# Kernel tuning notes

Measured on AMD Instinct MI355X. Metric: run time of the kernel, lower is better.

## Reference

```python
import jax, jax.numpy as jnp
import numpy as np

BINS = 10
MOMENTUM = 0.5


def setup_inputs() -> dict:
    key = jax.random.key(0)
    k1, k2 = jax.random.split(key)
    B, D = 4096, 512
    x = jax.random.normal(k1, (B, D), dtype=jnp.float32)
    targets = jax.random.randint(k2, (B,), 0, 100, dtype=jnp.int64)
    acc_sum = jnp.zeros((BINS,), dtype=jnp.float32)
    return {"x": x, "acc_sum": acc_sum, "targets": targets}


def reference(x, acc_sum, targets):
    bins, momentum = BINS, MOMENTUM
    B = x.shape[0]
    # bin edges: arange(bins+1)/bins, last edge bumped by 1e-6
    edges = jnp.arange(bins + 1, dtype=jnp.float32) / bins
    edges = edges.at[-1].add(1e-6)

    # F.normalize: x / max(||x||_2, 1e-12) row-wise
    norm = jnp.maximum(jnp.linalg.norm(x, axis=1, keepdims=True), 1e-12)
    xn = x / norm
    cos = xn @ xn.T  # [B, B]

    label = (targets[:, None] == targets[None, :]).astype(jnp.float32)  # [B, B]

    g = jnp.abs(cos - label).ravel()  # gradient-density statistic, in [0, 2]
    # bin index i such that edges[i] <= g < edges[i+1]
    idx = jnp.searchsorted(edges, g, side="right") - 1
    valid = (idx >= 0) & (idx < bins)  # g >= edges[-1] falls in no bin -> weight 0

    # fused histogram (replaces the 10-iteration mask loop)
    counts = jnp.bincount(jnp.where(valid, idx, bins), length=bins + 1)[:bins]
    counts = counts.astype(jnp.float32)

    tot = jnp.float32(B * B)
    acc_new = momentum * acc_sum + (1.0 - momentum) * counts  # EMA update (momentum > 0 path)
    w_bin = tot / (acc_new + 1e-6)  # per-bin weight

    weights = jnp.where(valid, w_bin[jnp.clip(idx, 0, bins - 1)], 0.0)
    valid_num = jnp.sum(counts)
    weights = jnp.where(valid_num > 0, weights / valid_num, weights)

    loss = jnp.mean((label.ravel() - cos.ravel()) ** 2 * weights)
    return loss
```

## Files before the change

kernel.cpp:

```cpp
#include <hip/hip_runtime.h>
#include <hip/hip_bf16.h>

typedef __bf16 bf16x8 __attribute__((ext_vector_type(8)));
typedef float f32x16 __attribute__((ext_vector_type(16)));

typedef __attribute__((address_space(1))) void GAS;
typedef __attribute__((address_space(3))) void LAS;
#define GLOAD16(gp, lp) __builtin_amdgcn_global_load_lds((GAS*)(gp), (LAS*)(lp), 16, 0, 0)

#define NB 4096
#define NDU 1024
#define NKT 16

__global__ __launch_bounds__(256) void nrm_split_k(const float* __restrict__ x,
                                                   __bf16* __restrict__ u,
                                                   float* __restrict__ stats) {
    if (blockIdx.x == 0 && threadIdx.x < 21) stats[threadIdx.x] = 0.0f;
    const int wid = threadIdx.x >> 6, lane = threadIdx.x & 63;
    const int row = blockIdx.x * 4 + wid;
    const float4* xr = reinterpret_cast<const float4*>(x + (size_t)row * 512);
    float4 v0 = xr[lane * 2 + 0];
    float4 v1 = xr[lane * 2 + 1];
    float xv[8] = {v0.x, v0.y, v0.z, v0.w, v1.x, v1.y, v1.z, v1.w};
    float ss = 0.0f;
#pragma unroll
    for (int j = 0; j < 8; ++j) ss += xv[j] * xv[j];
#pragma unroll
    for (int off = 32; off > 0; off >>= 1) ss += __shfl_xor(ss, off);
    const float rn = 1.0f / fmaxf(sqrtf(ss), 1e-12f);
    bf16x8 h, l;
#pragma unroll
    for (int j = 0; j < 8; ++j) {
        float xn = xv[j] * rn;
        __bf16 hb = (__bf16)xn;
        h[j] = hb;
        l[j] = (__bf16)(xn - (float)hb);
    }
    reinterpret_cast<bf16x8*>(u + (size_t)row * NDU)[lane] = h;
    reinterpret_cast<bf16x8*>(u + (size_t)row * NDU + 512)[lane] = l;
}

__global__ __launch_bounds__(512, 2) void gemm_stat_k(const __bf16* __restrict__ u,
                                                      const int* __restrict__ targets,
                                                      const float* __restrict__ acc_sum,
                                                      float* __restrict__ stats,
                                                      float* __restrict__ out) {
    __shared__ __align__(16) __bf16 lds[2][4][128 * 64];
    __shared__ int tgtR[256], tgtC[256];
    __shared__ float red_s[8][10], red_c[8][10];

    const int bid = blockIdx.x;
    const int swz = (bid & 7) * 32 + (bid >> 3);
    const int by = swz >> 4, bx = swz & 15;
    const int row0 = by * 256, col0 = bx * 256;
    const int tid = threadIdx.x, lane = tid & 63;
    const int wid = tid >> 6, wr = wid >> 2, wc = wid & 3;

    if (tid < 256) tgtR[tid] = targets[row0 + tid];
    else           tgtC[tid - 256] = targets[col0 + tid - 256];

    const int c0 = tid, c1 = tid + 512;
    const int r0c = c0 >> 3, x0 = ((c0 & 7) ^ (r0c & 7)) * 8;
    const int r1c = c1 >> 3, x1 = ((c1 & 7) ^ (r1c & 7)) * 8;

    auto STAGE = [&](int g) {
        const int kt = g >> 2, h = g & 3;
        const int slot = kt & 1, kcol = kt * 64;
        const int brow = ((h < 2) ? row0 : col0) + (h & 1) * 128;
        __bf16* dst = &lds[slot][h][0];
        GLOAD16(u + (size_t)(brow + r0c) * NDU + kcol + x0, dst + c0 * 8);
        GLOAD16(u + (size_t)(brow + r1c) * NDU + kcol + x1, dst + c1 * 8);
    };

    const int l31 = lane & 31, hi2 = lane >> 5;
    int rowAe[4], rowBe[2], colE[4];
#pragma unroll
    for (int m = 0; m < 4; ++m) rowAe[m] = (m * 32 + l31) * 64;
#pragma unroll
    for (int n = 0; n < 2; ++n) rowBe[n] = ((wc & 1) * 64 + n * 32 + l31) * 64;
#pragma unroll
    for (int ks = 0; ks < 4; ++ks) colE[ks] = (ks * 16 + hi2 * 8) ^ ((lane & 7) << 3);

    const f32x16 fz = {0,0,0,0, 0,0,0,0, 0,0,0,0, 0,0,0,0};
    f32x16 acc[4][2];
#pragma unroll
    for (int m = 0; m < 4; ++m)
#pragma unroll
        for (int n = 0; n < 2; ++n) acc[m][n] = fz;

    STAGE(0); STAGE(1); STAGE(2); STAGE(3); STAGE(4);
    asm volatile("s_waitcnt vmcnt(2)" ::: "memory");
    __builtin_amdgcn_s_barrier();
    __builtin_amdgcn_sched_barrier(0);

    for (int kt = 0; kt < NKT; ++kt) {
        const int slot = kt & 1;
        const __bf16* lA = &lds[slot][wr][0];
        const __bf16* lB = &lds[slot][2 + (wc >> 1)][0];
#pragma unroll
        for (int f = 0; f < 2; ++f) {
            bf16x8 af[4][2], bf[2][2];
#pragma unroll
            for (int kq = 0; kq < 2; ++kq) {
                const int ks = 2 * f + kq;
#pragma unroll
                for (int m = 0; m < 4; ++m)
                    af[m][kq] = *reinterpret_cast<const bf16x8*>(lA + rowAe[m] + colE[ks]);
#pragma unroll
                for (int n = 0; n < 2; ++n)
                    bf[n][kq] = *reinterpret_cast<const bf16x8*>(lB + rowBe[n] + colE[ks]);
            }
            {
                const int g = 4 * kt + 2 * f + 5;
                if (g < 4 * NKT) STAGE(g);
                if (g + 1 < 4 * NKT) STAGE(g + 1);
            }
            __builtin_amdgcn_s_barrier();
            __builtin_amdgcn_sched_barrier(0);
            __builtin_amdgcn_s_setprio(1);
#pragma unroll
            for (int kq = 0; kq < 2; ++kq)
#pragma unroll
                for (int m = 0; m < 4; ++m)
#pragma unroll
                    for (int n = 0; n < 2; ++n)
                        acc[m][n] = __builtin_amdgcn_mfma_f32_32x32x16_bf16(
                            af[m][kq], bf[n][kq], acc[m][n], 0, 0, 0);
            __builtin_amdgcn_s_setprio(0);
            __builtin_amdgcn_sched_barrier(0);
            if (f == 1) {
                if (kt < NKT - 2)       asm volatile("s_waitcnt vmcnt(2)" ::: "memory");
                else if (kt == NKT - 2) asm volatile("s_waitcnt vmcnt(0)" ::: "memory");
            }
            __builtin_amdgcn_s_barrier();
            __builtin_amdgcn_sched_barrier(0);
        }
    }

    int tcv[2];
#pragma unroll
    for (int n = 0; n < 2; ++n) tcv[n] = tgtC[wc * 64 + n * 32 + l31];

    constexpr float E[11] = {0.0f, 0.1f, 0.2f, 0.3f, 0.4f, 0.5f,
                             0.6f, 0.7f, 0.8f, 0.9f, 1.0f + 1e-6f};
    float sacc[10], cacc[10];
#pragma unroll
    for (int b = 0; b < 10; ++b) { sacc[b] = 0.0f; cacc[b] = 0.0f; }

#pragma unroll
    for (int m = 0; m < 4; ++m) {
        const int rbase = wr * 128 + m * 32 + hi2 * 4;
        int trv[16];
#pragma unroll
        for (int reg = 0; reg < 16; ++reg)
            trv[reg] = tgtR[rbase + (reg >> 2) * 8 + (reg & 3)];
#pragma unroll
        for (int n = 0; n < 2; ++n) {
            f32x16 v = acc[m][n];
            const int tc = tcv[n];
#pragma unroll
            for (int reg = 0; reg < 16; ++reg) {
                const float label = (trv[reg] == tc) ? 1.0f : 0.0f;
                const float g = fabsf(v[reg] - label);
                const float g2 = g * g;
                bool prev = true;
#pragma unroll
                for (int b = 0; b < 10; ++b) {
                    const bool ge = (g >= E[b + 1]);
                    const bool in = prev && (!ge);
                    sacc[b] += in ? g2 : 0.0f;
                    cacc[b] += in ? 1.0f : 0.0f;
                    prev = ge;
                }
            }
        }
    }

#pragma unroll
    for (int b = 0; b < 10; ++b) {
        float sv = sacc[b], cv = cacc[b];
#pragma unroll
        for (int off = 32; off > 0; off >>= 1) {
            sv += __shfl_xor(sv, off);
            cv += __shfl_xor(cv, off);
        }
        if (lane == 0) { red_s[wid][b] = sv; red_c[wid][b] = cv; }
    }
    __syncthreads();
    if (tid < 10) {
        float s = 0.0f, c = 0.0f;
#pragma unroll
        for (int w = 0; w < 8; ++w) { s += red_s[w][tid]; c += red_c[w][tid]; }
        atomicAdd(&stats[tid], s);
        atomicAdd(&stats[10 + tid], c);
        __threadfence();
    }
    __syncthreads();

    if (tid == 0) {
        int old = atomicAdd((int*)&stats[20], 1);
        if (old == 255) {
            __threadfence();
            const float tot = 16777216.0f;
            double num = 0.0, valid = 0.0;
#pragma unroll
            for (int b = 0; b < 10; ++b) {
                float sb = atomicAdd(&stats[b], 0.0f);
                float cnt = atomicAdd(&stats[10 + b], 0.0f);
                float accn = 0.5f * acc_sum[b] + 0.5f * cnt;
                float w = tot / (accn + 1e-6f);
                num += (double)sb * (double)w;
                valid += (double)cnt;
            }
            out[0] = (valid > 0.0) ? (float)(num / valid / 16777216.0) : 0.0f;
        }
    }
}

extern "C" void kernel_launch(void* const* d_in, const int* in_sizes, int n_in,
                              void* d_out, int out_size, void* d_ws, size_t ws_size,
                              hipStream_t stream) {
    const float* x = (const float*)d_in[0];
    const float* acc_sum = (const float*)d_in[1];
    const int* targets = (const int*)d_in[2];
    float* out = (float*)d_out;

    char* ws = (char*)d_ws;
    __bf16* u = (__bf16*)ws;
    float* stats = (float*)(ws + (size_t)NB * NDU * sizeof(__bf16));

    nrm_split_k<<<NB / 4, 256, 0, stream>>>(x, u, stats);
    gemm_stat_k<<<256, 512, 0, stream>>>(u, targets, acc_sum, stats, out);
}
```

Measured before the change: 161.9 us.

## Simplify GEMM pipeline to one-tile-ahead prefetch with single barrier per k-step

Replaces the fine-grained quarter-tile staging schedule (five stages in flight, two barriers per half-iteration, setprio and sched_barrier hints) with a simple double-buffer. The whole next k-tile is issued at the top of each iteration and followed by a full vmcnt(0) wait and one barrier at the end. It also precomputes base pointers so each stage is eight loads with constant offsets. This cuts barrier and address-arithmetic overhead, but prefetch depth drops and the scheduling hints that interleaved MFMA with loads are gone, so load latency may be exposed.

Result: no change. 162.2 us (+0.2%).

```diff
diff --git a/kernel.cpp b/kernel.cpp
--- a/kernel.cpp
+++ b/kernel.cpp
@@ -59,27 +59,31 @@
     if (tid < 256) tgtR[tid] = targets[row0 + tid];
     else           tgtC[tid - 256] = targets[col0 + tid - 256];
 
-    const int c0 = tid, c1 = tid + 512;
-    const int r0c = c0 >> 3, x0 = ((c0 & 7) ^ (r0c & 7)) * 8;
-    const int r1c = c1 >> 3, x1 = ((c1 & 7) ^ (r1c & 7)) * 8;
-
-    auto STAGE = [&](int g) {
-        const int kt = g >> 2, h = g & 3;
-        const int slot = kt & 1, kcol = kt * 64;
-        const int brow = ((h < 2) ? row0 : col0) + (h & 1) * 128;
-        __bf16* dst = &lds[slot][h][0];
-        GLOAD16(u + (size_t)(brow + r0c) * NDU + kcol + x0, dst + c0 * 8);
-        GLOAD16(u + (size_t)(brow + r1c) * NDU + kcol + x1, dst + c1 * 8);
+    const int r0c = tid >> 3;
+    const int x0 = ((tid & 7) ^ (r0c & 7)) * 8;
+    const __bf16* A0 = u + (size_t)(row0 + r0c) * NDU + x0;
+    const __bf16* B0 = u + (size_t)(col0 + r0c) * NDU + x0;
+    const int de0 = tid * 8, de1 = tid * 8 + 4096;
+
+    auto STAGE = [&](int kt) {
+        const int slot = kt & 1, kc = kt * 64;
+        GLOAD16(A0 + kc,             &lds[slot][0][de0]);
+        GLOAD16(A0 + kc +  64 * NDU, &lds[slot][0][de1]);
+        GLOAD16(A0 + kc + 128 * NDU, &lds[slot][1][de0]);
+        GLOAD16(A0 + kc + 192 * NDU, &lds[slot][1][de1]);
+        GLOAD16(B0 + kc,             &lds[slot][2][de0]);
+        GLOAD16(B0 + kc +  64 * NDU, &lds[slot][2][de1]);
+        GLOAD16(B0 + kc + 128 * NDU, &lds[slot][3][de0]);
+        GLOAD16(B0 + kc + 192 * NDU, &lds[slot][3][de1]);
     };
 
     const int l31 = lane & 31, hi2 = lane >> 5;
-    int rowAe[4], rowBe[2], colE[4];
+    const int xr_ = (lane & 7) << 3;
+    int rowAe[4], rowBe[2];
 #pragma unroll
     for (int m = 0; m < 4; ++m) rowAe[m] = (m * 32 + l31) * 64;
 #pragma unroll
     for (int n = 0; n < 2; ++n) rowBe[n] = ((wc & 1) * 64 + n * 32 + l31) * 64;
-#pragma unroll
-    for (int ks = 0; ks < 4; ++ks) colE[ks] = (ks * 16 + hi2 * 8) ^ ((lane & 7) << 3);
 
     const f32x16 fz = {0,0,0,0, 0,0,0,0, 0,0,0,0, 0,0,0,0};
     f32x16 acc[4][2];
@@ -88,53 +92,34 @@
 #pragma unroll
         for (int n = 0; n < 2; ++n) acc[m][n] = fz;
 
-    STAGE(0); STAGE(1); STAGE(2); STAGE(3); STAGE(4);
-    asm volatile("s_waitcnt vmcnt(2)" ::: "memory");
+    STAGE(0);
+    asm volatile("s_waitcnt vmcnt(0)" ::: "memory");
     __builtin_amdgcn_s_barrier();
-    __builtin_amdgcn_sched_barrier(0);
 
     for (int kt = 0; kt < NKT; ++kt) {
+        if (kt + 1 < NKT) STAGE(kt + 1);
         const int slot = kt & 1;
         const __bf16* lA = &lds[slot][wr][0];
         const __bf16* lB = &lds[slot][2 + (wc >> 1)][0];
 #pragma unroll
-        for (int f = 0; f < 2; ++f) {
-            bf16x8 af[4][2], bf[2][2];
-#pragma unroll
-            for (int kq = 0; kq < 2; ++kq) {
-                const int ks = 2 * f + kq;
-#pragma unroll
-                for (int m = 0; m < 4; ++m)
-                    af[m][kq] = *reinterpret_cast<const bf16x8*>(lA + rowAe[m] + colE[ks]);
+        for (int ks = 0; ks < 4; ++ks) {
+            const int ce = (ks * 16 + hi2 * 8) ^ xr_;
+            bf16x8 af[4], bf[2];
+#pragma unroll
+            for (int m = 0; m < 4; ++m)
+                af[m] = *reinterpret_cast<const bf16x8*>(lA + rowAe[m] + ce);
+#pragma unroll
+            for (int n = 0; n < 2; ++n)
+                bf[n] = *reinterpret_cast<const bf16x8*>(lB + rowBe[n] + ce);
+#pragma unroll
+            for (int m = 0; m < 4; ++m)
 #pragma unroll
                 for (int n = 0; n < 2; ++n)
-                    bf[n][kq] = *reinterpret_cast<const bf16x8*>(lB + rowBe[n] + colE[ks]);
-            }
-            {
-                const int g = 4 * kt + 2 * f + 5;
-                if (g < 4 * NKT) STAGE(g);
-                if (g + 1 < 4 * NKT) STAGE(g + 1);
-            }
-            __builtin_amdgcn_s_barrier();
-            __builtin_amdgcn_sched_barrier(0);
-            __builtin_amdgcn_s_setprio(1);
-#pragma unroll
-            for (int kq = 0; kq < 2; ++kq)
-#pragma unroll
-                for (int m = 0; m < 4; ++m)
-#pragma unroll
-                    for (int n = 0; n < 2; ++n)
-                        acc[m][n] = __builtin_amdgcn_mfma_f32_32x32x16_bf16(
-                            af[m][kq], bf[n][kq], acc[m][n], 0, 0, 0);
-            __builtin_amdgcn_s_setprio(0);
-            __builtin_amdgcn_sched_barrier(0);
-            if (f == 1) {
-                if (kt < NKT - 2)       asm volatile("s_waitcnt vmcnt(2)" ::: "memory");
-                else if (kt == NKT - 2) asm volatile("s_waitcnt vmcnt(0)" ::: "memory");
-            }
-            __builtin_amdgcn_s_barrier();
-            __builtin_amdgcn_sched_barrier(0);
-        }
+                    acc[m][n] = __builtin_amdgcn_mfma_f32_32x32x16_bf16(
+                        af[m], bf[n], acc[m][n], 0, 0, 0);
+        }
+        asm volatile("s_waitcnt vmcnt(0)" ::: "memory");
+        __builtin_amdgcn_s_barrier();
     }
 
     int tcv[2];
```
